# Kernel tuning notes

Hardware: AMD Instinct MI355X
Metric: run time of the kernel (lower is better)

## Reference

```python
import jax, jax.numpy as jnp
import numpy as np

EPS = 1e-5
RATE = 0.5

def _ln(x, g, b):
    m = jnp.mean(x, axis=-1, keepdims=True)
    v = jnp.mean((x - m) ** 2, axis=-1, keepdims=True)
    return (x - m) * jax.lax.rsqrt(v + EPS) * g + b

def _attn(xq, xk, xv, Wq, Wk, Wv, Wo, num_heads, rate):
    B, Lq, _ = xq.shape
    Lk = xk.shape[1]
    q = (xq @ Wq).reshape(B, Lq, num_heads, -1).transpose(0, 2, 1, 3)  # b h q d
    k = (xk @ Wk).reshape(B, Lk, num_heads, -1).transpose(0, 2, 1, 3)
    v = (xv @ Wv).reshape(B, Lk, num_heads, -1).transpose(0, 2, 1, 3)
    d = q.shape[-1]
    scores = jnp.einsum('bhqd,bhkd->bhqk', q, k) / jnp.sqrt(jnp.float32(d))
    p = jax.nn.softmax(scores, axis=-1)
    # non-standard gating: keep softmax weight only where sigmoid(score) > rate
    p = jnp.where(jax.nn.sigmoid(scores) > rate, p, jnp.zeros_like(p))
    o = jnp.einsum('bhqk,bhkd->bhqd', p, v)
    o = o.transpose(0, 2, 1, 3).reshape(B, Lq, -1)
    return o @ Wo

def setup_inputs() -> dict:
    key = jax.random.key(0)
    ks = jax.random.split(key, 16)
    D, Z, H = 512, 100, 512  # query_size, zelta feat dim, num_hiddens
    s = 0.02
    inp = {
        'X': jax.random.normal(ks[0], (4, 2048, D), jnp.float32),
        'Zelta': jax.random.normal(ks[1], (4, 1024, Z), jnp.float32),
        'Wq_s': jax.random.normal(ks[2], (D, H), jnp.float32) * s,
        'Wk_s': jax.random.normal(ks[3], (D, H), jnp.float32) * s,
        'Wv_s': jax.random.normal(ks[4], (D, H), jnp.float32) * s,
        'Wo_s': jax.random.normal(ks[5], (H, D), jnp.float32) * s,
        'Wq_c': jax.random.normal(ks[6], (D, H), jnp.float32) * s,
        'Wk_c': jax.random.normal(ks[7], (Z, 512), jnp.float32) * s,
        'Wv_c': jax.random.normal(ks[8], (Z, 512), jnp.float32) * s,
        'Wo_c': jax.random.normal(ks[9], (H, D), jnp.float32) * s,
        'g1': jnp.ones((D,), jnp.float32),
        'b1': jnp.zeros((D,), jnp.float32),
        'g2': jnp.ones((Z,), jnp.float32),
        'b2': jnp.zeros((Z,), jnp.float32),
        'W1': jax.random.normal(ks[10], (D, H), jnp.float32) * s,
        'bf1': jnp.zeros((H,), jnp.float32),
        'W2': jax.random.normal(ks[11], (H, D), jnp.float32) * s,
        'bf2': jnp.zeros((D,), jnp.float32),
    }
    return inp

def reference(X, Zelta, Wq_s, Wk_s, Wv_s, Wo_s, Wq_c, Wk_c, Wv_c, Wo_c,
              g1, b1, g2, b2, W1, bf1, W2, bf2):
    # dropout layers are identity in eval mode
    n = _ln(X, g1, b1)
    X = X + _attn(n, n, n, Wq_s, Wk_s, Wv_s, Wo_s, 8, RATE)
    n = _ln(X, g1, b1)
    zn = _ln(Zelta, g2, b2)
    X = X + _attn(n, zn, zn, Wq_c, Wk_c, Wv_c, Wo_c, 8, RATE)
    n = _ln(X, g1, b1)
    h = jax.nn.gelu(n @ W1 + bf1, approximate=False)
    X = X + (h @ W2 + bf2)
    return X
```

## Files before the change

kernel.cpp:

```cpp
#include <hip/hip_runtime.h>
#include <hip/hip_bf16.h>
#include <cstdint>

typedef unsigned short u16;
typedef short s16x8 __attribute__((ext_vector_type(8)));
typedef float f32x4 __attribute__((ext_vector_type(4)));

#define AS1 __attribute__((address_space(1)))
#define AS3 __attribute__((address_space(3)))

#define QSCALE 0.18033688011112042f

#if __has_builtin(__builtin_amdgcn_exp2f)
#define EXP2(x) __builtin_amdgcn_exp2f(x)
#else
#define EXP2(x) __expf((x) * 0.6931471805599453f)
#endif

__device__ __forceinline__ u16 f2bf(float f) {
    union { float f; unsigned int u; } x; x.f = f;
    unsigned int r = (x.u + 0x7FFFu + ((x.u >> 16) & 1u)) >> 16;
    return (u16)r;
}

__device__ __forceinline__ float bf2f(u16 u) {
    union { unsigned int u; float f; } x; x.u = ((unsigned)u) << 16;
    return x.f;
}

__device__ __forceinline__ unsigned fbits(float f) {
    union { float f; unsigned int u; } x; x.f = f;
    return x.u;
}

__device__ __forceinline__ unsigned pack_bf2r(float a, float b) {
    return ((fbits(a) + 0x8000u) >> 16) | ((fbits(b) + 0x8000u) & 0xffff0000u);
}

struct WPtrs { const float* s[8]; u16* d[8]; };

__global__ void wt_batch(WPtrs p, int K, int N, int Kp) {
    int idx = blockIdx.x * 256 + threadIdx.x;
    if (idx >= N * Kp) return;
    int n = idx / Kp, k = idx - n * Kp;
    const float* W = p.s[blockIdx.y];
    float v = (k < K) ? W[(size_t)k * N + n] : 0.f;
    p.d[blockIdx.y][idx] = f2bf(v);
}

__global__ __launch_bounds__(256)
void ln512(const float* __restrict__ X, const float* __restrict__ g,
           const float* __restrict__ bta, u16* __restrict__ out) {
    const int lane = threadIdx.x & 63, w = threadIdx.x >> 6;
    const long row = (long)blockIdx.x * 4 + w;
    const float* xp = X + row * 512 + lane * 8;
    f32x4 a = *(const f32x4*)xp;
    f32x4 c = *(const f32x4*)(xp + 4);
    float s = 0.f, ss = 0.f;
#pragma unroll
    for (int i = 0; i < 4; i++) { s += a[i] + c[i]; ss += a[i]*a[i] + c[i]*c[i]; }
#pragma unroll
    for (int m = 1; m < 64; m <<= 1) { s += __shfl_xor(s, m); ss += __shfl_xor(ss, m); }
    float mean = s * (1.f / 512.f);
    float var  = ss * (1.f / 512.f) - mean * mean;
    float rs = rsqrtf(var + 1e-5f);
    f32x4 g0 = *(const f32x4*)(g + lane * 8);
    f32x4 g1 = *(const f32x4*)(g + lane * 8 + 4);
    f32x4 b0 = *(const f32x4*)(bta + lane * 8);
    f32x4 b1 = *(const f32x4*)(bta + lane * 8 + 4);
    s16x8 ov;
#pragma unroll
    for (int i = 0; i < 4; i++) {
        ov[i]     = (short)f2bf((a[i] - mean) * rs * g0[i] + b0[i]);
        ov[4 + i] = (short)f2bf((c[i] - mean) * rs * g1[i] + b1[i]);
    }
    *(s16x8*)&out[row * 512 + lane * 8] = ov;
}

__global__ __launch_bounds__(256)
void ln_z(const float* __restrict__ Z, const float* __restrict__ g,
          const float* __restrict__ bta, u16* __restrict__ out) {
    const int lane = threadIdx.x & 63, w = threadIdx.x >> 6;
    const long row = (long)blockIdx.x * 4 + w;
    const float* zp = Z + row * 100;
    float x0 = zp[lane];
    float x1 = (lane < 36) ? zp[64 + lane] : 0.f;
    float s = x0 + x1, ss = x0 * x0 + x1 * x1;
#pragma unroll
    for (int m = 1; m < 64; m <<= 1) { s += __shfl_xor(s, m); ss += __shfl_xor(ss, m); }
    float mean = s * 0.01f;
    float var  = ss * 0.01f - mean * mean;
    float rs = rsqrtf(var + 1e-5f);
    out[row * 128 + lane] = f2bf((x0 - mean) * rs * g[lane] + bta[lane]);
    u16 hi = 0;
    if (lane < 36) hi = f2bf((x1 - mean) * rs * g[64 + lane] + bta[64 + lane]);
    out[row * 128 + 64 + lane] = hi;
}

template <int BM, int BN, int EPI>
__global__ __launch_bounds__(256)
void gemm_p(const u16* __restrict__ A, const u16* __restrict__ BT,
            void* __restrict__ Outv, void* __restrict__ Outv2,
            const float* __restrict__ bias, const float* __restrict__ res,
            int M, int N, int K) {
    __shared__ u16 Ash[2][BM * 32];
    __shared__ u16 Bsh[2][BN * 32];
    constexpr int MR = BM / 32;
    constexpr int NR = BN / 32;
    constexpr int ROUNDS = (BM + BN) / 64;
    const int tid = threadIdx.x;
    const int lane = tid & 63, w = tid >> 6;
    const int wm = w >> 1, wn = w & 1;
    const int lr = lane & 15, lg = lane >> 4;
    const int seg = lane & 3;
    const long m0 = (long)blockIdx.y * BM, n0 = (long)blockIdx.x * BN;

    f32x4 acc[MR][NR];
#pragma unroll
    for (int i = 0; i < MR; i++)
#pragma unroll
        for (int j = 0; j < NR; j++) { f32x4 z = {0.f, 0.f, 0.f, 0.f}; acc[i][j] = z; }

    auto stage = [&](int buf, int kk) {
        const long k0 = (long)kk * 32;
#pragma unroll
        for (int rd = 0; rd < ROUNDS; rd++) {
            const int rbase = rd * 64 + w * 16;
            const int r = rbase + (lane >> 2);
            if (rbase < BM) {
                __builtin_amdgcn_global_load_lds(
                    (const AS1 void*)(A + (m0 + r) * K + k0 + seg * 8),
                    (AS3 void*)(&Ash[buf][rbase * 32]), 16, 0, 0);
            } else {
                __builtin_amdgcn_global_load_lds(
                    (const AS1 void*)(BT + (n0 + r - BM) * K + k0 + seg * 8),
                    (AS3 void*)(&Bsh[buf][(rbase - BM) * 32]), 16, 0, 0);
            }
        }
    };

    const int ksteps = K >> 5;
    stage(0, 0);
    __syncthreads();
    int cur = 0;
    for (int kk = 0; kk < ksteps; ++kk) {
        if (kk + 1 < ksteps) stage(cur ^ 1, kk + 1);
        s16x8 af[MR], bf[NR];
#pragma unroll
        for (int mi = 0; mi < MR; mi++)
            af[mi] = *(const s16x8*)&Ash[cur][(wm * (BM / 2) + mi * 16 + lr) * 32 + lg * 8];
#pragma unroll
        for (int ni = 0; ni < NR; ni++)
            bf[ni] = *(const s16x8*)&Bsh[cur][(wn * (BN / 2) + ni * 16 + lr) * 32 + lg * 8];
#pragma unroll
        for (int mi = 0; mi < MR; mi++)
#pragma unroll
            for (int ni = 0; ni < NR; ni++)
                acc[mi][ni] = __builtin_amdgcn_mfma_f32_16x16x32_bf16(af[mi], bf[ni], acc[mi][ni], 0, 0, 0);
        __syncthreads();
        cur ^= 1;
    }
#pragma unroll
    for (int mi = 0; mi < MR; mi++) {
#pragma unroll
        for (int ni = 0; ni < NR; ni++) {
#pragma unroll
            for (int r = 0; r < 4; r++) {
                long gm = m0 + wm * (BM / 2) + mi * 16 + lg * 4 + r;
                long gn = n0 + wn * (BN / 2) + ni * 16 + lr;
                float v = acc[mi][ni][r];
                if constexpr (EPI == 1) {
                    v += bias[gn];
                    v = 0.5f * v * (1.f + erff(v * 0.70710678118654752f));
                    ((u16*)Outv)[gm * (long)N + gn] = f2bf(v);
                } else if constexpr (EPI == 2) {
                    if (bias) v += bias[gn];
                    v += res[gm * (long)N + gn];
                    ((float*)Outv)[gm * (long)N + gn] = v;
                } else if constexpr (EPI == 3) {
                    ((u16*)Outv)[gm * (long)N + gn] = f2bf(v * QSCALE);
                } else if constexpr (EPI == 4) {
                    if (gn < 512) ((u16*)Outv)[gm * 512 + gn] = f2bf(v * QSCALE);
                    else          ((u16*)Outv2)[gm * 512 + (gn - 512)] = f2bf(v);
                } else {
                    ((u16*)Outv)[gm * (long)N + gn] = f2bf(v);
                }
            }
        }
    }
}

__global__ __launch_bounds__(256)
void attn_gated6(const u16* __restrict__ Q, const u16* __restrict__ Kp,
                 const u16* __restrict__ VT, u16* __restrict__ OP,
                 float* __restrict__ PS, int Lq, int Lk, int Tk, int TT) {
    __shared__ u16 Kt[2][2048];
    __shared__ u16 Vt[2][2048];
    __shared__ u16 Psh[4][2][640];
    const int tid = threadIdx.x, lane = tid & 63, w = tid >> 6;
    const int lr = lane & 15, lg = lane >> 4;

    const int nx = gridDim.x, ny = gridDim.y;
    int id = blockIdx.x + nx * (blockIdx.y + ny * blockIdx.z);
    int qq = (nx * ny * gridDim.z) >> 3;
    int r2 = (id & 7) * qq + (id >> 3);
    int bx = r2 % nx; int t1 = r2 / nx; int by = t1 % ny; int bz = t1 / ny;

    const int b = by >> 3, h = by & 7;
    const long qrow0 = (long)b * Lq + (long)bx * 128 + w * 32;
    const int hoff = h * 64;
    const int Lkh = Lk >> 1;

    s16x8 qf[2][2];
#pragma unroll
    for (int s = 0; s < 2; s++)
#pragma unroll
        for (int dc = 0; dc < 2; dc++)
            qf[s][dc] = *(const s16x8*)&Q[(qrow0 + s * 16 + lr) * 512 + hoff + dc * 32 + lg * 8];

    f32x4 o[2][4];
#pragma unroll
    for (int s = 0; s < 2; s++)
#pragma unroll
        for (int dt = 0; dt < 4; dt++) { f32x4 z = {0.f, 0.f, 0.f, 0.f}; o[s][dt] = z; }
    float psum[2] = {0.f, 0.f};

    const int krow = tid >> 3, kp = tid & 7;
    const u16* ksrc = Kp + ((long)b * Lk + (long)bz * Lkh + krow) * 512
                         + hoff + ((kp ^ (krow & 7)) * 8);
    const int vrow = tid >> 2, vc = tid & 3;
    const u16* vsrc = VT + (long)(hoff + vrow) * Tk + (long)b * Lk
                         + (long)bz * Lkh + vc * 8;

    auto stage = [&](int buf) {
        __builtin_amdgcn_global_load_lds((const AS1 void*)ksrc,
                                         (AS3 void*)(&Kt[buf][w * 512]), 16, 0, 0);
        __builtin_amdgcn_global_load_lds((const AS1 void*)vsrc,
                                         (AS3 void*)(&Vt[buf][w * 512]), 16, 0, 0);
        ksrc += 32 * 512;
        vsrc += 32;
    };

    const int steps = Lkh >> 5;
    stage(0);
    __syncthreads();
    int cur = 0;
    for (int it = 0; it < steps; ++it) {
        if (it + 1 < steps) stage(cur ^ 1);
        s16x8 kf[2][2], vb[4];
#pragma unroll
        for (int c = 0; c < 2; c++)
#pragma unroll
            for (int dc = 0; dc < 2; dc++)
                kf[c][dc] = *(const s16x8*)&Kt[cur][(c * 16 + lr) * 64 + (((dc * 4 + lg) ^ (lr & 7)) * 8)];
#pragma unroll
        for (int dt = 0; dt < 4; dt++)
            vb[dt] = *(const s16x8*)&Vt[cur][(dt * 16 + lr) * 32 + lg * 8];
#pragma unroll
        for (int s = 0; s < 2; s++) {
            f32x4 st[2];
            { f32x4 z = {0.f, 0.f, 0.f, 0.f}; st[0] = z; st[1] = z; }
#pragma unroll
            for (int c = 0; c < 2; c++)
#pragma unroll
                for (int dc = 0; dc < 2; dc++)
                    st[c] = __builtin_amdgcn_mfma_f32_16x16x32_bf16(kf[c][dc], qf[s][dc], st[c], 0, 0, 0);
            uint2 pk[2];
#pragma unroll
            for (int c = 0; c < 2; c++) {
                float e0 = EXP2(st[c][0]), e1 = EXP2(st[c][1]);
                float e2 = EXP2(st[c][2]), e3 = EXP2(st[c][3]);
                psum[s] += (e0 + e1) + (e2 + e3);
                float g0 = st[c][0] > 0.f ? e0 : 0.f;
                float g1 = st[c][1] > 0.f ? e1 : 0.f;
                float g2 = st[c][2] > 0.f ? e2 : 0.f;
                float g3 = st[c][3] > 0.f ? e3 : 0.f;
                pk[c].x = pack_bf2r(g0, g1);
                pk[c].y = pack_bf2r(g2, g3);
            }
            u16* psh = &Psh[w][s][0];
#pragma unroll
            for (int c = 0; c < 2; c++)
                *(uint2*)&psh[lr * 40 + c * 16 + lg * 4] = pk[c];
            s16x8 pa = *(const s16x8*)&psh[lr * 40 + lg * 8];
#pragma unroll
            for (int dt = 0; dt < 4; dt++)
                o[s][dt] = __builtin_amdgcn_mfma_f32_16x16x32_bf16(pa, vb[dt], o[s][dt], 0, 0, 0);
        }
        __syncthreads();
        cur ^= 1;
    }

    u16* op = OP + (long)bz * TT * 512;
    float* ps = PS + (long)bz * TT * 8;
#pragma unroll
    for (int s = 0; s < 2; s++) {
        float red = psum[s];
        red += __shfl_xor(red, 16);
        red += __shfl_xor(red, 32);
        if (lg == 0) ps[(qrow0 + s * 16 + lr) * 8 + h] = red;
#pragma unroll
        for (int dt = 0; dt < 4; dt++) {
            long ob = (qrow0 + s * 16) * 512 + hoff + dt * 16 + lr;
            op[ob + (long)(lg * 4 + 0) * 512] = f2bf(o[s][dt][0]);
            op[ob + (long)(lg * 4 + 1) * 512] = f2bf(o[s][dt][1]);
            op[ob + (long)(lg * 4 + 2) * 512] = f2bf(o[s][dt][2]);
            op[ob + (long)(lg * 4 + 3) * 512] = f2bf(o[s][dt][3]);
        }
    }
}

__global__ __launch_bounds__(256)
void attn_combine(const u16* __restrict__ OP, const float* __restrict__ PS,
                  u16* __restrict__ O, int TT) {
    long i = (long)blockIdx.x * 256 + threadIdx.x;
    long t = i >> 6; int g = (int)(i & 63); int d0 = g * 8; int h = g >> 3;
    float rinv = 1.f / (PS[t * 8 + h] + PS[(long)TT * 8 + t * 8 + h]);
    s16x8 va = *(const s16x8*)&OP[t * 512 + d0];
    s16x8 vb = *(const s16x8*)&OP[(long)TT * 512 + t * 512 + d0];
    s16x8 ov;
#pragma unroll
    for (int j = 0; j < 8; j++)
        ov[j] = (short)f2bf((bf2f((u16)va[j]) + bf2f((u16)vb[j])) * rinv);
    *(s16x8*)&O[t * 512 + d0] = ov;
}

extern "C" void kernel_launch(void* const* d_in, const int* in_sizes, int n_in,
                              void* d_out, int out_size, void* d_ws, size_t ws_size,
                              hipStream_t stream) {
    const float* X    = (const float*)d_in[0];
    const float* Z    = (const float*)d_in[1];
    const float* Wq_s = (const float*)d_in[2];
    const float* Wk_s = (const float*)d_in[3];
    const float* Wv_s = (const float*)d_in[4];
    const float* Wo_s = (const float*)d_in[5];
    const float* Wq_c = (const float*)d_in[6];
    const float* Wk_c = (const float*)d_in[7];
    const float* Wv_c = (const float*)d_in[8];
    const float* Wo_c = (const float*)d_in[9];
    const float* g1   = (const float*)d_in[10];
    const float* b1   = (const float*)d_in[11];
    const float* g2   = (const float*)d_in[12];
    const float* b2   = (const float*)d_in[13];
    const float* W1   = (const float*)d_in[14];
    const float* bf1  = (const float*)d_in[15];
    const float* W2   = (const float*)d_in[16];
    const float* bf2  = (const float*)d_in[17];
    float* out = (float*)d_out;
    const int TT = 8192;

    char* p = (char*)d_ws;
    auto take = [&](size_t n) { char* q = p; p += (n + 255) & ~(size_t)255; return q; };
    u16* WqkT = (u16*)take((size_t)2 * 512 * 512 * 2);
    u16* WqsT = WqkT;
    u16* WksT = WqkT + 512 * 512;
    u16* WvsT = (u16*)take(512 * 512 * 2);
    u16* WosT = (u16*)take(512 * 512 * 2);
    u16* WqcT = (u16*)take(512 * 512 * 2);
    u16* WocT = (u16*)take(512 * 512 * 2);
    u16* W1T  = (u16*)take(512 * 512 * 2);
    u16* W2T  = (u16*)take(512 * 512 * 2);
    u16* WkcT = (u16*)take(512 * 128 * 2);
    u16* WvcT = (u16*)take(512 * 128 * 2);
    u16* nbuf = (u16*)take((size_t)TT * 512 * 2);
    u16* qbuf = (u16*)take((size_t)TT * 512 * 2);
    u16* kbuf = (u16*)take((size_t)TT * 512 * 2);
    u16* vtbuf = (u16*)take((size_t)TT * 512 * 2);
    u16* abuf = (u16*)take((size_t)TT * 512 * 2);
    u16* znb  = (u16*)take((size_t)4096 * 128 * 2);
    u16* opart = (u16*)take((size_t)2 * TT * 512 * 2);
    float* psum = (float*)take((size_t)2 * TT * 8 * 4);

    WPtrs w8{};
    w8.s[0] = Wq_s; w8.d[0] = WqsT;
    w8.s[1] = Wk_s; w8.d[1] = WksT;
    w8.s[2] = Wv_s; w8.d[2] = WvsT;
    w8.s[3] = Wo_s; w8.d[3] = WosT;
    w8.s[4] = Wq_c; w8.d[4] = WqcT;
    w8.s[5] = Wo_c; w8.d[5] = WocT;
    w8.s[6] = W1;   w8.d[6] = W1T;
    w8.s[7] = W2;   w8.d[7] = W2T;
    wt_batch<<<dim3(1024, 8), 256, 0, stream>>>(w8, 512, 512, 512);
    WPtrs w2{};
    w2.s[0] = Wk_c; w2.d[0] = WkcT;
    w2.s[1] = Wv_c; w2.d[1] = WvcT;
    wt_batch<<<dim3(256, 2), 256, 0, stream>>>(w2, 100, 512, 128);

    ln512<<<2048, 256, 0, stream>>>(X, g1, b1, nbuf);
    gemm_p<128, 64, 4><<<dim3(16, 64), 256, 0, stream>>>(nbuf, WqkT, qbuf, kbuf, nullptr, nullptr, 8192, 1024, 512);
    gemm_p<64, 128, 0><<<dim3(64, 8), 256, 0, stream>>>(WvsT, nbuf, vtbuf, nullptr, nullptr, nullptr, 512, 8192, 512);
    attn_gated6<<<dim3(16, 32, 2), 256, 0, stream>>>(qbuf, kbuf, vtbuf, opart, psum, 2048, 2048, 8192, TT);
    attn_combine<<<2048, 256, 0, stream>>>(opart, psum, abuf, TT);
    gemm_p<128, 64, 2><<<dim3(8, 64), 256, 0, stream>>>(abuf, WosT, d_out, nullptr, nullptr, X, 8192, 512, 512);

    ln512<<<2048, 256, 0, stream>>>(out, g1, b1, nbuf);
    ln_z<<<1024, 256, 0, stream>>>(Z, g2, b2, znb);
    gemm_p<128, 64, 3><<<dim3(8, 64), 256, 0, stream>>>(nbuf, WqcT, qbuf, nullptr, nullptr, nullptr, 8192, 512, 512);
    gemm_p<128, 64, 0><<<dim3(8, 32), 256, 0, stream>>>(znb, WkcT, kbuf, nullptr, nullptr, nullptr, 4096, 512, 128);
    gemm_p<64, 128, 0><<<dim3(32, 8), 256, 0, stream>>>(WvcT, znb, vtbuf, nullptr, nullptr, nullptr, 512, 4096, 128);
    attn_gated6<<<dim3(16, 32, 2), 256, 0, stream>>>(qbuf, kbuf, vtbuf, opart, psum, 2048, 1024, 4096, TT);
    attn_combine<<<2048, 256, 0, stream>>>(opart, psum, abuf, TT);
    gemm_p<128, 64, 2><<<dim3(8, 64), 256, 0, stream>>>(abuf, WocT, d_out, nullptr, nullptr, out, 8192, 512, 512);

    ln512<<<2048, 256, 0, stream>>>(out, g1, b1, nbuf);
    gemm_p<128, 64, 1><<<dim3(8, 64), 256, 0, stream>>>(nbuf, W1T, abuf, nullptr, bf1, nullptr, 8192, 512, 512);
    gemm_p<128, 64, 2><<<dim3(8, 64), 256, 0, stream>>>(abuf, W2T, d_out, nullptr, bf2, out, 8192, 512, 512);
}
```

Measured before the change: 375.6 us.

## Triple-buffer GEMM and attention LDS pipelines with explicit vmcnt waits and priority hints

Switches the GEMM and gated-attention kernels from double to triple buffering in shared memory, prefetching two stages ahead. The full __syncthreads is replaced by explicit s_waitcnt vmcnt counts plus s_barrier, and MFMA sections are bracketed with s_setprio hints. The weight transpose kernel is also rewritten to use a 64x64 shared-memory tile so both its reads and writes are coalesced. This costs more LDS, which may lower occupancy, and hard-coded vmcnt literals depend on an exact count of loads per stage.

```diff
diff --git a/kernel.cpp b/kernel.cpp
--- a/kernel.cpp
+++ b/kernel.cpp
@@ -17,6 +17,10 @@
 #define EXP2(x) __expf((x) * 0.6931471805599453f)
 #endif
 
+#define VMCNT(n) asm volatile("s_waitcnt vmcnt(" #n ")" ::: "memory")
+#define BARRIER() do { __builtin_amdgcn_s_barrier(); \
+                       __builtin_amdgcn_sched_barrier(0); } while (0)
+
 __device__ __forceinline__ u16 f2bf(float f) {
     union { float f; unsigned int u; } x; x.f = f;
     unsigned int r = (x.u + 0x7FFFu + ((x.u >> 16) & 1u)) >> 16;
@@ -39,13 +43,24 @@
 
 struct WPtrs { const float* s[8]; u16* d[8]; };
 
-__global__ void wt_batch(WPtrs p, int K, int N, int Kp) {
-    int idx = blockIdx.x * 256 + threadIdx.x;
-    if (idx >= N * Kp) return;
-    int n = idx / Kp, k = idx - n * Kp;
-    const float* W = p.s[blockIdx.y];
-    float v = (k < K) ? W[(size_t)k * N + n] : 0.f;
-    p.d[blockIdx.y][idx] = f2bf(v);
+__global__ __launch_bounds__(256)
+void wt_batch(WPtrs p, int K, int N, int Kp) {
+    __shared__ float t[64][65];
+    const int tx = threadIdx.x & 63, ty = threadIdx.x >> 6;
+    const int k0 = blockIdx.x * 64, n0 = blockIdx.y * 64;
+    const float* W = p.s[blockIdx.z];
+    u16* D = p.d[blockIdx.z];
+#pragma unroll
+    for (int i = 0; i < 16; i++) {
+        int k = i * 4 + ty;
+        t[k][tx] = (k0 + k < K) ? W[(size_t)(k0 + k) * N + n0 + tx] : 0.f;
+    }
+    __syncthreads();
+#pragma unroll
+    for (int i = 0; i < 16; i++) {
+        int n = i * 4 + ty;
+        D[(size_t)(n0 + n) * Kp + k0 + tx] = f2bf(t[tx][n]);
+    }
 }
 
 __global__ __launch_bounds__(256)
@@ -103,11 +118,12 @@
             void* __restrict__ Outv, void* __restrict__ Outv2,
             const float* __restrict__ bias, const float* __restrict__ res,
             int M, int N, int K) {
-    __shared__ u16 Ash[2][BM * 32];
-    __shared__ u16 Bsh[2][BN * 32];
+    __shared__ u16 Ash[3][BM * 32];
+    __shared__ u16 Bsh[3][BN * 32];
     constexpr int MR = BM / 32;
     constexpr int NR = BN / 32;
     constexpr int ROUNDS = (BM + BN) / 64;
+    static_assert(ROUNDS == 3, "vmcnt literals assume 3 loads per stage");
     const int tid = threadIdx.x;
     const int lane = tid & 63, w = tid >> 6;
     const int wm = w >> 1, wn = w & 1;
@@ -141,10 +157,12 @@
 
     const int ksteps = K >> 5;
     stage(0, 0);
-    __syncthreads();
-    int cur = 0;
+    stage(1, 1);
+    VMCNT(3);
+    BARRIER();
+    int cur = 0, nb = 2;
     for (int kk = 0; kk < ksteps; ++kk) {
-        if (kk + 1 < ksteps) stage(cur ^ 1, kk + 1);
+        if (kk + 2 < ksteps) stage(nb, kk + 2);
         s16x8 af[MR], bf[NR];
 #pragma unroll
         for (int mi = 0; mi < MR; mi++)
@@ -152,13 +170,18 @@
 #pragma unroll
         for (int ni = 0; ni < NR; ni++)
             bf[ni] = *(const s16x8*)&Bsh[cur][(wn * (BN / 2) + ni * 16 + lr) * 32 + lg * 8];
+        __builtin_amdgcn_s_setprio(1);
 #pragma unroll
         for (int mi = 0; mi < MR; mi++)
 #pragma unroll
             for (int ni = 0; ni < NR; ni++)
                 acc[mi][ni] = __builtin_amdgcn_mfma_f32_16x16x32_bf16(af[mi], bf[ni], acc[mi][ni], 0, 0, 0);
-        __syncthreads();
-        cur ^= 1;
+        __builtin_amdgcn_s_setprio(0);
+        if (kk + 2 < ksteps) { VMCNT(3); }
+        else                 { VMCNT(0); }
+        BARRIER();
+        cur = (cur == 2) ? 0 : cur + 1;
+        nb  = (nb == 2) ? 0 : nb + 1;
     }
 #pragma unroll
     for (int mi = 0; mi < MR; mi++) {
@@ -191,11 +214,11 @@
 }
 
 __global__ __launch_bounds__(256)
-void attn_gated6(const u16* __restrict__ Q, const u16* __restrict__ Kp,
+void attn_gated7(const u16* __restrict__ Q, const u16* __restrict__ Kp,
                  const u16* __restrict__ VT, u16* __restrict__ OP,
                  float* __restrict__ PS, int Lq, int Lk, int Tk, int TT) {
-    __shared__ u16 Kt[2][2048];
-    __shared__ u16 Vt[2][2048];
+    __shared__ u16 Kt[3][2048];
+    __shared__ u16 Vt[3][2048];
     __shared__ u16 Psh[4][2][640];
     const int tid = threadIdx.x, lane = tid & 63, w = tid >> 6;
     const int lr = lane & 15, lg = lane >> 4;
@@ -243,10 +266,12 @@
 
     const int steps = Lkh >> 5;
     stage(0);
-    __syncthreads();
-    int cur = 0;
+    stage(1);
+    VMCNT(2);
+    BARRIER();
+    int cur = 0, nb = 2;
     for (int it = 0; it < steps; ++it) {
-        if (it + 1 < steps) stage(cur ^ 1);
+        if (it + 2 < steps) stage(nb);
         s16x8 kf[2][2], vb[4];
 #pragma unroll
         for (int c = 0; c < 2; c++)
@@ -260,11 +285,13 @@
         for (int s = 0; s < 2; s++) {
             f32x4 st[2];
             { f32x4 z = {0.f, 0.f, 0.f, 0.f}; st[0] = z; st[1] = z; }
+            __builtin_amdgcn_s_setprio(1);
 #pragma unroll
             for (int c = 0; c < 2; c++)
 #pragma unroll
                 for (int dc = 0; dc < 2; dc++)
                     st[c] = __builtin_amdgcn_mfma_f32_16x16x32_bf16(kf[c][dc], qf[s][dc], st[c], 0, 0, 0);
+            __builtin_amdgcn_s_setprio(0);
             uint2 pk[2];
 #pragma unroll
             for (int c = 0; c < 2; c++) {
@@ -283,12 +310,17 @@
             for (int c = 0; c < 2; c++)
                 *(uint2*)&psh[lr * 40 + c * 16 + lg * 4] = pk[c];
             s16x8 pa = *(const s16x8*)&psh[lr * 40 + lg * 8];
+            __builtin_amdgcn_s_setprio(1);
 #pragma unroll
             for (int dt = 0; dt < 4; dt++)
                 o[s][dt] = __builtin_amdgcn_mfma_f32_16x16x32_bf16(pa, vb[dt], o[s][dt], 0, 0, 0);
+            __builtin_amdgcn_s_setprio(0);
         }
-        __syncthreads();
-        cur ^= 1;
+        if (it + 2 < steps) { VMCNT(2); }
+        else                { VMCNT(0); }
+        BARRIER();
+        cur = (cur == 2) ? 0 : cur + 1;
+        nb  = (nb == 2) ? 0 : nb + 1;
     }
 
     u16* op = OP + (long)bz * TT * 512;
@@ -380,16 +412,16 @@
     w8.s[5] = Wo_c; w8.d[5] = WocT;
     w8.s[6] = W1;   w8.d[6] = W1T;
     w8.s[7] = W2;   w8.d[7] = W2T;
-    wt_batch<<<dim3(1024, 8), 256, 0, stream>>>(w8, 512, 512, 512);
+    wt_batch<<<dim3(8, 8, 8), 256, 0, stream>>>(w8, 512, 512, 512);
     WPtrs w2{};
     w2.s[0] = Wk_c; w2.d[0] = WkcT;
     w2.s[1] = Wv_c; w2.d[1] = WvcT;
-    wt_batch<<<dim3(256, 2), 256, 0, stream>>>(w2, 100, 512, 128);
+    wt_batch<<<dim3(2, 8, 2), 256, 0, stream>>>(w2, 100, 512, 128);
 
     ln512<<<2048, 256, 0, stream>>>(X, g1, b1, nbuf);
     gemm_p<128, 64, 4><<<dim3(16, 64), 256, 0, stream>>>(nbuf, WqkT, qbuf, kbuf, nullptr, nullptr, 8192, 1024, 512);
     gemm_p<64, 128, 0><<<dim3(64, 8), 256, 0, stream>>>(WvsT, nbuf, vtbuf, nullptr, nullptr, nullptr, 512, 8192, 512);
-    attn_gated6<<<dim3(16, 32, 2), 256, 0, stream>>>(qbuf, kbuf, vtbuf, opart, psum, 2048, 2048, 8192, TT);
+    attn_gated7<<<dim3(16, 32, 2), 256, 0, stream>>>(qbuf, kbuf, vtbuf, opart, psum, 2048, 2048, 8192, TT);
     attn_combine<<<2048, 256, 0, stream>>>(opart, psum, abuf, TT);
     gemm_p<128, 64, 2><<<dim3(8, 64), 256, 0, stream>>>(abuf, WosT, d_out, nullptr, nullptr, X, 8192, 512, 512);
 
@@ -398,7 +430,7 @@
     gemm_p<128, 64, 3><<<dim3(8, 64), 256, 0, stream>>>(nbuf, WqcT, qbuf, nullptr, nullptr, nullptr, 8192, 512, 512);
     gemm_p<128, 64, 0><<<dim3(8, 32), 256, 0, stream>>>(znb, WkcT, kbuf, nullptr, nullptr, nullptr, 4096, 512, 128);
     gemm_p<64, 128, 0><<<dim3(32, 8), 256, 0, stream>>>(WvcT, znb, vtbuf, nullptr, nullptr, nullptr, 512, 4096, 128);
-    attn_gated6<<<dim3(16, 32, 2), 256, 0, stream>>>(qbuf, kbuf, vtbuf, opart, psum, 2048, 1024, 4096, TT);
+    attn_gated7<<<dim3(16, 32, 2), 256, 0, stream>>>(qbuf, kbuf, vtbuf, opart, psum, 2048, 1024, 4096, TT);
     attn_combine<<<2048, 256, 0, stream>>>(opart, psum, abuf, TT);
     gemm_p<128, 64, 2><<<dim3(8, 64), 256, 0, stream>>>(abuf, WocT, d_out, nullptr, nullptr, out, 8192, 512, 512);
 
```

New measurement: 377.5 us. No clear change (+0.5%).
